# Optimization experiments

Measured on AMD Instinct MI355X. Metric: run time of the kernel, lower is better.

Reference implementation:

```python
import jax, jax.numpy as jnp
import numpy as np

B, T = 2, 5            # num_frames MUST equal 5 (Embedding(5, channel) pos table)
C, CTX_C, DH = 384, 128, 64   # channel, context_channel, dim_head (lucidrains default, heads=1)
HW = [(80, 80), (40, 40), (20, 20), (10, 10)]
NS = 4
SCALE = DH ** -0.5


def _xavier(k, shape):
    fan_out, fan_in = shape[-2], shape[-1]
    lim = (6.0 / (fan_in + fan_out)) ** 0.5
    return jax.random.uniform(k, shape, jnp.float32, -lim, lim)


def setup_inputs() -> dict:
    key = jax.random.key(0)
    ks = iter(jax.random.split(key, 40))
    inp = {}
    for i, (h, w) in enumerate(HW):
        inp[f"fmap{i}"] = jax.random.normal(next(ks), (B * T, C, h, w), jnp.float32)
        inp[f"pos{i}"] = jax.random.normal(next(ks), (B, T, C, h, w), jnp.float32)
        inp[f"audio{i}"] = jax.random.normal(next(ks), (B * T, CTX_C), jnp.float32)
    inp["ctx_proj_w"] = _xavier(next(ks), (NS, C, CTX_C))
    inp["ctx_proj_b"] = jnp.zeros((NS, C), jnp.float32)
    inp["pos_emb"] = jax.random.normal(next(ks), (NS, 5, C), jnp.float32)  # Embedding(5, channel) per stage
    inp["qk_w"] = _xavier(next(ks), (NS, DH, C))
    inp["ctx_qk_w"] = _xavier(next(ks), (NS, DH, C))
    inp["v_w"] = _xavier(next(ks), (NS, DH, C))
    inp["ctx_v_w"] = _xavier(next(ks), (NS, DH, C))
    inp["out_w"] = _xavier(next(ks), (NS, C, DH))
    inp["out_b"] = jnp.zeros((NS, C), jnp.float32)
    inp["ctx_out_w"] = _xavier(next(ks), (NS, C, DH))
    inp["ctx_out_b"] = jnp.zeros((NS, C), jnp.float32)
    inp["batch_size"] = B
    inp["num_frames"] = T
    return inp


def _stage(x, pos, audio, Wp, bp, pe, Wqk, Wcqk, Wv, Wcv, Wo, bo, Wco, bco, batch_size):
    bt, c, h, w = x.shape
    # audio projection 128 -> 384
    a = audio @ Wp.T + bp                                  # (bt, C)
    # 'hw' reshape: tokens = H*W per (batch*frame)
    xf = x.reshape(bt, c, h * w).transpose(0, 2, 1)        # (bt, hw, C)
    vp = pos.reshape(bt, c, h * w).transpose(0, 2, 1)      # (bt, hw, C)
    ctx = a[:, None, :]                                    # (bt, 1, C)
    cp = jnp.tile(pe, (batch_size, 1))[:, None, :]         # (bt, 1, C); bt == 5*batch_size
    # bidirectional cross-attention (heads=1), pos added to QK inputs only
    qk = (xf + vp) @ Wqk.T                                 # (bt, hw, DH)
    v = xf @ Wv.T                                          # (bt, hw, DH)
    cqk = (ctx + cp) @ Wcqk.T                              # (bt, 1, DH)
    cv = ctx @ Wcv.T                                       # (bt, 1, DH)
    sim = jnp.einsum('bid,bjd->bij', qk, cqk) * SCALE      # (bt, hw, 1) shared similarity
    attn = jax.nn.softmax(sim, axis=-1)                    # video attends over context (j)
    ctx_attn = jax.nn.softmax(sim, axis=-2)                # context attends over video (i)
    out = jnp.einsum('bij,bjd->bid', attn, cv) @ Wo.T + bo         # (bt, hw, C)
    ctx_out = jnp.einsum('bij,bid->bjd', ctx_attn, v) @ Wco.T + bco  # (bt, 1, C)
    vout = out.transpose(0, 2, 1).reshape(bt, c, h, w)
    aout = ctx_out[:, 0, :]                                # (bt, C)
    return vout, aout


def reference(fmap0, fmap1, fmap2, fmap3, audio0, audio1, audio2, audio3,
              pos0, pos1, pos2, pos3,
              ctx_proj_w, ctx_proj_b, pos_emb, qk_w, ctx_qk_w, v_w, ctx_v_w,
              out_w, out_b, ctx_out_w, ctx_out_b, batch_size, num_frames):
    fmaps = (fmap0, fmap1, fmap2, fmap3)
    poss = (pos0, pos1, pos2, pos3)
    audios = (audio0, audio1, audio2, audio3)
    vouts, aouts = [], []
    for i in range(NS):
        vo, ao = _stage(fmaps[i], poss[i], audios[i],
                        ctx_proj_w[i], ctx_proj_b[i], pos_emb[i],
                        qk_w[i], ctx_qk_w[i], v_w[i], ctx_v_w[i],
                        out_w[i], out_b[i], ctx_out_w[i], ctx_out_b[i], batch_size)
        vouts.append(vo)
        aouts.append(ao)
    return tuple(vouts) + tuple(aouts)
```

## Files before the change

kernel.cpp:

```cpp
#include <hip/hip_runtime.h>

#define BT 10
#define CC 384
#define DH 64
#define CTXC 128
#define NS 4
#define SCALE_F 0.125f

#define VOFF0 0
#define VOFF1 24576000
#define VOFF2 30720000
#define VOFF3 32256000
#define AOUT_OFF 32640000
#define SIM_TOT 85000

struct Params {
  const float* fmap0; const float* fmap1; const float* fmap2; const float* fmap3;
  const float* pos0;  const float* pos1;  const float* pos2;  const float* pos3;
  const float* audio0;const float* audio1;const float* audio2;const float* audio3;
  const float* ctx_proj_w; const float* ctx_proj_b; const float* pos_emb;
  const float* qk_w; const float* ctx_qk_w; const float* v_w; const float* ctx_v_w;
  const float* out_w; const float* out_b; const float* ctx_out_w; const float* ctx_out_b;
  float* out;
  float* r;
  float* outvec;
  float* xw;
  float* simbuf;
};

__device__ __forceinline__ int hw_of(int s){ return s==0?6400: s==1?1600: s==2?400:100; }
__device__ __forceinline__ int simoff(int s){ return s==0?0: s==1?64000: s==2?80000:84000; }
__device__ __forceinline__ size_t voutoff(int s){ return s==0?(size_t)VOFF0: s==1?(size_t)VOFF1: s==2?(size_t)VOFF2:(size_t)VOFF3; }
__device__ __forceinline__ const float* fm_of(const Params& P, int s){ return s==0?P.fmap0: s==1?P.fmap1: s==2?P.fmap2:P.fmap3; }
__device__ __forceinline__ const float* po_of(const Params& P, int s){ return s==0?P.pos0: s==1?P.pos1: s==2?P.pos2:P.pos3; }
__device__ __forceinline__ const float* au_of(const Params& P, int s){ return s==0?P.audio0: s==1?P.audio1: s==2?P.audio2:P.audio3; }

__global__ __launch_bounds__(384) void k_pre(Params P) {
  const int s = blockIdx.x / BT, b = blockIdx.x % BT;
  const int tid = threadIdx.x;
  __shared__ float aud[CTXC], ctxv[CC], ctxpe[CC], cqk[DH], cvv[DH];
  const float* audio = au_of(P, s);
  if (tid < CTXC) aud[tid] = audio[b*CTXC + tid];
  __syncthreads();
  {
    float acc = P.ctx_proj_b[s*CC + tid];
    const float* wrow = P.ctx_proj_w + (size_t)(s*CC + tid)*CTXC;
    #pragma unroll 8
    for (int k = 0; k < CTXC; ++k) acc += wrow[k]*aud[k];
    ctxv[tid] = acc;
    ctxpe[tid] = acc + P.pos_emb[(s*5 + (b%5))*CC + tid];
  }
  __syncthreads();
  if (tid < DH) {
    float q = 0.f, v = 0.f;
    const float* wq = P.ctx_qk_w + (size_t)(s*DH + tid)*CC;
    const float* wv = P.ctx_v_w  + (size_t)(s*DH + tid)*CC;
    #pragma unroll 4
    for (int c = 0; c < CC; ++c) { q += wq[c]*ctxpe[c]; v += wv[c]*ctxv[c]; }
    cqk[tid] = q; cvv[tid] = v;
  }
  __syncthreads();
  {
    float rr = 0.f, ov = P.out_b[s*CC + tid];
    const float* wqk = P.qk_w + (size_t)s*DH*CC + tid;
    const float* wo  = P.out_w + (size_t)(s*CC + tid)*DH;
    #pragma unroll 4
    for (int d = 0; d < DH; ++d) { rr += wqk[(size_t)d*CC]*cqk[d]; ov += wo[d]*cvv[d]; }
    P.r[(s*BT+b)*CC + tid] = rr * SCALE_F;
    P.outvec[(s*BT+b)*CC + tid] = ov;
  }
}

__global__ __launch_bounds__(128) void k_fill(Params P) {
  const int row = blockIdx.x;
  const int s = row / 3840, local = row % 3840;
  const int HW = hw_of(s);
  const float val = P.outvec[s*3840 + local];
  float* dst = P.out + voutoff(s) + (size_t)local*HW;
  const float4 v4 = {val, val, val, val};
  for (int i = threadIdx.x*4; i < HW; i += 128*4)
    *(float4*)(dst + i) = v4;
}

__global__ __launch_bounds__(256) void k_sim(Params P) {
  int bid = blockIdx.x;
  const int part = (bid >= 350) ? 1 : 0;
  bid -= part*350;
  int s, local, cb, HW;
  if (bid < 250)      { s=0; local=bid;      cb=25; HW=6400; }
  else if (bid < 320) { s=1; local=bid-250;  cb=7;  HW=1600; }
  else if (bid < 340) { s=2; local=bid-320;  cb=2;  HW=400;  }
  else                { s=3; local=bid-340;  cb=1;  HW=100;  }
  const int b = local / cb, chunk = local % cb;
  const int tid = threadIdx.x;
  const int c0 = part * 192;

  __shared__ float rs[192];
  const float* rrow = P.r + (s*BT+b)*CC + c0;
  if (tid < 192) rs[tid] = rrow[tid];
  __syncthreads();

  const int i = chunk*256 + tid;
  if (i < HW) {
    const float* xp = fm_of(P, s) + ((size_t)b*CC + c0)*HW + i;
    const float* pp = po_of(P, s) + ((size_t)b*CC + c0)*HW + i;
    float acc = 0.f;
    #pragma unroll 8
    for (int c = 0; c < 192; ++c)
      acc += (xp[(size_t)c*HW] + pp[(size_t)c*HW]) * rs[c];
    P.simbuf[part*SIM_TOT + simoff(s) + b*HW + i] = acc;
  }
}

__global__ __launch_bounds__(256) void k_softmax(Params P) {
  const int s = blockIdx.x / BT, b = blockIdx.x % BT;
  const int HW = hw_of(s);
  float* sim  = P.simbuf + simoff(s) + b*HW;
  const float* sim2 = sim + SIM_TOT;
  const int tid = threadIdx.x;
  const int wid = tid >> 6, lane = tid & 63;
  __shared__ float red[4], red2[4];

  float m = -1e30f;
  for (int i = tid; i < HW; i += 256) { float v = sim[i] + sim2[i]; sim[i] = v; m = fmaxf(m, v); }
  #pragma unroll
  for (int off = 32; off; off >>= 1) m = fmaxf(m, __shfl_down(m, off));
  if (lane == 0) red[wid] = m;
  __syncthreads();
  if (tid == 0) { float mm = red[0]; for (int w2 = 1; w2 < 4; ++w2) mm = fmaxf(mm, red[w2]); red[0] = mm; }
  __syncthreads();
  m = red[0];

  float sum = 0.f;
  for (int i = tid; i < HW; i += 256) sum += expf(sim[i] - m);
  #pragma unroll
  for (int off = 32; off; off >>= 1) sum += __shfl_down(sum, off);
  if (lane == 0) red2[wid] = sum;
  __syncthreads();
  if (tid == 0) { float ss = red2[0]; for (int w2 = 1; w2 < 4; ++w2) ss += red2[w2]; red2[0] = ss; }
  __syncthreads();
  const float invS = 1.f / red2[0];

  for (int i = tid; i < HW; i += 256) sim[i] = expf(sim[i] - m) * invS;
}

__global__ __launch_bounds__(256) void k_xw(Params P) {
  const int bid = blockIdx.x;
  const int sb = bid / 96, ct = bid % 96;
  const int s = sb / BT, b = sb % BT;
  const int HW = hw_of(s);
  const int wid = threadIdx.x >> 6, lane = threadIdx.x & 63;
  const int c = ct*4 + wid;
  const float* xrow = fm_of(P, s) + ((size_t)(b*CC + c))*HW;
  const float* wrow = P.simbuf + simoff(s) + b*HW;
  float ax=0.f, ay=0.f, az=0.f, aw=0.f;
  #pragma unroll 4
  for (int i0 = lane*4; i0 < HW; i0 += 256) {
    const float4 x4 = *(const float4*)(xrow + i0);
    const float4 w4 = *(const float4*)(wrow + i0);
    ax += x4.x*w4.x; ay += x4.y*w4.y; az += x4.z*w4.z; aw += x4.w*w4.w;
  }
  float acc = (ax + ay) + (az + aw);
  #pragma unroll
  for (int off = 32; off; off >>= 1) acc += __shfl_down(acc, off);
  if (lane == 0) P.xw[(s*BT+b)*CC + c] = acc;
}

__global__ __launch_bounds__(384) void k_post(Params P) {
  const int s = blockIdx.x / BT, b = blockIdx.x % BT;
  const int tid = threadIdx.x;
  __shared__ float xws[CC], ctxo[DH];
  xws[tid] = P.xw[(s*BT+b)*CC + tid];
  __syncthreads();
  if (tid < DH) {
    float acc = 0.f;
    const float* wv = P.v_w + (size_t)(s*DH + tid)*CC;
    #pragma unroll 4
    for (int c = 0; c < CC; ++c) acc += wv[c]*xws[c];
    ctxo[tid] = acc;
  }
  __syncthreads();
  float ao = P.ctx_out_b[s*CC + tid];
  const float* wco = P.ctx_out_w + (size_t)(s*CC + tid)*DH;
  #pragma unroll 4
  for (int d = 0; d < DH; ++d) ao += wco[d]*ctxo[d];
  P.out[(size_t)AOUT_OFF + (s*BT+b)*CC + tid] = ao;
}

extern "C" void kernel_launch(void* const* d_in, const int* in_sizes, int n_in,
                              void* d_out, int out_size, void* d_ws, size_t ws_size,
                              hipStream_t stream) {
  Params P;
  P.fmap0 = (const float*)d_in[0];  P.pos0 = (const float*)d_in[1];  P.audio0 = (const float*)d_in[2];
  P.fmap1 = (const float*)d_in[3];  P.pos1 = (const float*)d_in[4];  P.audio1 = (const float*)d_in[5];
  P.fmap2 = (const float*)d_in[6];  P.pos2 = (const float*)d_in[7];  P.audio2 = (const float*)d_in[8];
  P.fmap3 = (const float*)d_in[9];  P.pos3 = (const float*)d_in[10]; P.audio3 = (const float*)d_in[11];
  P.ctx_proj_w = (const float*)d_in[12]; P.ctx_proj_b = (const float*)d_in[13];
  P.pos_emb = (const float*)d_in[14];
  P.qk_w = (const float*)d_in[15];  P.ctx_qk_w = (const float*)d_in[16];
  P.v_w = (const float*)d_in[17];   P.ctx_v_w = (const float*)d_in[18];
  P.out_w = (const float*)d_in[19]; P.out_b = (const float*)d_in[20];
  P.ctx_out_w = (const float*)d_in[21]; P.ctx_out_b = (const float*)d_in[22];
  P.out = (float*)d_out;

  float* ws = (float*)d_ws;
  P.r      = ws;
  P.outvec = ws + 15360;
  P.xw     = ws + 30720;
  P.simbuf = ws + 46080;

  k_pre    <<<NS*BT, 384, 0, stream>>>(P);
  k_fill   <<<15360, 128, 0, stream>>>(P);
  k_sim    <<<700,   256, 0, stream>>>(P);
  k_softmax<<<NS*BT, 256, 0, stream>>>(P);
  k_xw     <<<3840,  256, 0, stream>>>(P);
  k_post   <<<NS*BT, 384, 0, stream>>>(P);
}
```

Measured before the change: 460.6 us.

## Split sim channel reduction 8-way with float4 loads and atomics; flatten fill

The similarity kernel now splits the 384-channel reduction into 8 parts of 48 channels instead of 2. Each thread processes four tokens using float4 loads, and partial sums are combined with atomicAdd into a zero-initialised buffer. This exposes more parallelism and wider memory accesses, at the cost of a memset and atomic contention. The softmax keeps the exponentials to avoid computing them twice, and the constant-fill kernel is flattened into one float4 store per thread and moved to the end of the launch sequence.

```diff
diff --git a/kernel.cpp b/kernel.cpp
--- a/kernel.cpp
+++ b/kernel.cpp
@@ -12,7 +12,6 @@
 #define VOFF2 30720000
 #define VOFF3 32256000
 #define AOUT_OFF 32640000
-#define SIM_TOT 85000
 
 struct Params {
   const float* fmap0; const float* fmap1; const float* fmap2; const float* fmap3;
@@ -30,7 +29,6 @@
 
 __device__ __forceinline__ int hw_of(int s){ return s==0?6400: s==1?1600: s==2?400:100; }
 __device__ __forceinline__ int simoff(int s){ return s==0?0: s==1?64000: s==2?80000:84000; }
-__device__ __forceinline__ size_t voutoff(int s){ return s==0?(size_t)VOFF0: s==1?(size_t)VOFF1: s==2?(size_t)VOFF2:(size_t)VOFF3; }
 __device__ __forceinline__ const float* fm_of(const Params& P, int s){ return s==0?P.fmap0: s==1?P.fmap1: s==2?P.fmap2:P.fmap3; }
 __device__ __forceinline__ const float* po_of(const Params& P, int s){ return s==0?P.pos0: s==1?P.pos1: s==2?P.pos2:P.pos3; }
 __device__ __forceinline__ const float* au_of(const Params& P, int s){ return s==0?P.audio0: s==1?P.audio1: s==2?P.audio2:P.audio3; }
@@ -71,58 +69,54 @@
   }
 }
 
-__global__ __launch_bounds__(128) void k_fill(Params P) {
-  const int row = blockIdx.x;
-  const int s = row / 3840, local = row % 3840;
-  const int HW = hw_of(s);
-  const float val = P.outvec[s*3840 + local];
-  float* dst = P.out + voutoff(s) + (size_t)local*HW;
-  const float4 v4 = {val, val, val, val};
-  for (int i = threadIdx.x*4; i < HW; i += 128*4)
-    *(float4*)(dst + i) = v4;
-}
-
 __global__ __launch_bounds__(256) void k_sim(Params P) {
-  int bid = blockIdx.x;
-  const int part = (bid >= 350) ? 1 : 0;
-  bid -= part*350;
-  int s, local, cb, HW;
-  if (bid < 250)      { s=0; local=bid;      cb=25; HW=6400; }
-  else if (bid < 320) { s=1; local=bid-250;  cb=7;  HW=1600; }
-  else if (bid < 340) { s=2; local=bid-320;  cb=2;  HW=400;  }
-  else                { s=3; local=bid-340;  cb=1;  HW=100;  }
-  const int b = local / cb, chunk = local % cb;
-  const int tid = threadIdx.x;
-  const int c0 = part * 192;
-
-  __shared__ float rs[192];
-  const float* rrow = P.r + (s*BT+b)*CC + c0;
-  if (tid < 192) rs[tid] = rrow[tid];
-  __syncthreads();
-
-  const int i = chunk*256 + tid;
-  if (i < HW) {
-    const float* xp = fm_of(P, s) + ((size_t)b*CC + c0)*HW + i;
-    const float* pp = po_of(P, s) + ((size_t)b*CC + c0)*HW + i;
-    float acc = 0.f;
+  const int bid = blockIdx.x;
+  int s, b, chunk, part, HW;
+  if (bid < 560)      { s=0; int l=bid;     b=l/56; int r2=l%56; chunk=r2>>3; part=r2&7; HW=6400; }
+  else if (bid < 720) { s=1; int l=bid-560; b=l/16; int r2=l%16; chunk=r2>>3; part=r2&7; HW=1600; }
+  else if (bid < 800) { s=2; int l=bid-720; b=l>>3; part=l&7; chunk=0; HW=400; }
+  else                { s=3; int l=bid-800; b=l>>3; part=l&7; chunk=0; HW=100; }
+  const int tid = threadIdx.x;
+  const int c0 = part*48;
+  const int hw4 = HW >> 2;
+
+  __shared__ float rs[48];
+  if (tid < 48) rs[tid] = P.r[(s*BT+b)*CC + c0 + tid];
+  __syncthreads();
+
+  const int i4 = chunk*256 + tid;
+  if (i4 < hw4) {
+    const float4* xp = (const float4*)(fm_of(P, s) + ((size_t)b*CC + c0)*HW) + i4;
+    const float4* pp = (const float4*)(po_of(P, s) + ((size_t)b*CC + c0)*HW) + i4;
+    float4 acc = {0.f, 0.f, 0.f, 0.f};
     #pragma unroll 8
-    for (int c = 0; c < 192; ++c)
-      acc += (xp[(size_t)c*HW] + pp[(size_t)c*HW]) * rs[c];
-    P.simbuf[part*SIM_TOT + simoff(s) + b*HW + i] = acc;
+    for (int c = 0; c < 48; ++c) {
+      const float4 x = xp[(size_t)c*hw4];
+      const float4 p = pp[(size_t)c*hw4];
+      const float rc = rs[c];
+      acc.x += (x.x + p.x) * rc;
+      acc.y += (x.y + p.y) * rc;
+      acc.z += (x.z + p.z) * rc;
+      acc.w += (x.w + p.w) * rc;
+    }
+    float* dst = P.simbuf + simoff(s) + b*HW + i4*4;
+    atomicAdd(dst + 0, acc.x);
+    atomicAdd(dst + 1, acc.y);
+    atomicAdd(dst + 2, acc.z);
+    atomicAdd(dst + 3, acc.w);
   }
 }
 
 __global__ __launch_bounds__(256) void k_softmax(Params P) {
   const int s = blockIdx.x / BT, b = blockIdx.x % BT;
   const int HW = hw_of(s);
-  float* sim  = P.simbuf + simoff(s) + b*HW;
-  const float* sim2 = sim + SIM_TOT;
+  float* sim = P.simbuf + simoff(s) + b*HW;
   const int tid = threadIdx.x;
   const int wid = tid >> 6, lane = tid & 63;
   __shared__ float red[4], red2[4];
 
   float m = -1e30f;
-  for (int i = tid; i < HW; i += 256) { float v = sim[i] + sim2[i]; sim[i] = v; m = fmaxf(m, v); }
+  for (int i = tid; i < HW; i += 256) m = fmaxf(m, sim[i]);
   #pragma unroll
   for (int off = 32; off; off >>= 1) m = fmaxf(m, __shfl_down(m, off));
   if (lane == 0) red[wid] = m;
@@ -132,7 +126,7 @@
   m = red[0];
 
   float sum = 0.f;
-  for (int i = tid; i < HW; i += 256) sum += expf(sim[i] - m);
+  for (int i = tid; i < HW; i += 256) { float e = expf(sim[i] - m); sim[i] = e; sum += e; }
   #pragma unroll
   for (int off = 32; off; off >>= 1) sum += __shfl_down(sum, off);
   if (lane == 0) red2[wid] = sum;
@@ -141,7 +135,7 @@
   __syncthreads();
   const float invS = 1.f / red2[0];
 
-  for (int i = tid; i < HW; i += 256) sim[i] = expf(sim[i] - m) * invS;
+  for (int i = tid; i < HW; i += 256) sim[i] *= invS;
 }
 
 __global__ __launch_bounds__(256) void k_xw(Params P) {
@@ -187,6 +181,22 @@
   P.out[(size_t)AOUT_OFF + (s*BT+b)*CC + tid] = ao;
 }
 
+template<int F4PR, int VOFF, int OVOFF>
+__device__ __forceinline__ void fill_one(const Params& P, int idx) {
+  const int row = idx / F4PR;
+  const float val = P.outvec[OVOFF + row];
+  const float4 v4 = {val, val, val, val};
+  ((float4*)(P.out + VOFF))[idx] = v4;
+}
+
+__global__ __launch_bounds__(256) void k_fill(Params P) {
+  const int gid = blockIdx.x * 256 + threadIdx.x;
+  if (blockIdx.x < 24000)      fill_one<1600, VOFF0, 0>    (P, gid);
+  else if (blockIdx.x < 30000) fill_one< 400, VOFF1, 3840> (P, gid - 24000*256);
+  else if (blockIdx.x < 31500) fill_one< 100, VOFF2, 7680> (P, gid - 30000*256);
+  else                         fill_one<  25, VOFF3, 11520>(P, gid - 31500*256);
+}
+
 extern "C" void kernel_launch(void* const* d_in, const int* in_sizes, int n_in,
                               void* d_out, int out_size, void* d_ws, size_t ws_size,
                               hipStream_t stream) {
@@ -209,10 +219,11 @@
   P.xw     = ws + 30720;
   P.simbuf = ws + 46080;
 
+  hipMemsetAsync(P.simbuf, 0, 85000*sizeof(float), stream);
   k_pre    <<<NS*BT, 384, 0, stream>>>(P);
-  k_fill   <<<15360, 128, 0, stream>>>(P);
-  k_sim    <<<700,   256, 0, stream>>>(P);
+  k_sim    <<<880,   256, 0, stream>>>(P);
   k_softmax<<<NS*BT, 256, 0, stream>>>(P);
   k_xw     <<<3840,  256, 0, stream>>>(P);
   k_post   <<<NS*BT, 384, 0, stream>>>(P);
-}
+  k_fill   <<<31875, 256, 0, stream>>>(P);
+}
```

Result: slower. 471.5 us (+2.4%).
